# Optimization experiments

Measured on AMD Instinct MI355X. Metric: run time of the kernel, lower is better.

The kernel has to match this reference:

```python
import jax, jax.numpy as jnp
import numpy as np

MARGIN = 0.3
EPS = 1e-12


def setup_inputs() -> dict:
    key = jax.random.key(0)
    k1, k2, k3 = jax.random.split(key, 3)
    B, D = 8192, 1024
    features = jax.random.normal(k1, (B, D), dtype=jnp.float32)
    labels = jax.random.randint(k2, (B,), 0, 100, dtype=jnp.int64)
    domain_labels = jax.random.randint(k3, (B,), 0, 2, dtype=jnp.int64)
    return {"features": features, "labels": labels, "domain_labels": domain_labels}


def reference(features, labels, domain_labels):
    # L2-normalize rows (F.normalize: x / max(||x||, eps))
    norm = jnp.maximum(jnp.linalg.norm(features, axis=1, keepdims=True), EPS)
    f = features / norm

    herb = domain_labels == 0   # [B] anchors
    field = domain_labels == 1  # [B] candidates

    sq = jnp.sum(f * f, axis=1)                                   # [B]
    d2 = sq[:, None] + sq[None, :] - 2.0 * jnp.einsum('id,jd->ij', f, f)
    d = jnp.sqrt(jnp.maximum(d2, 0.0))                            # [B, B]

    same = labels[:, None] == labels[None, :]                     # [B, B]
    pair = herb[:, None] & field[None, :]
    pos_mask = pair & same
    neg_mask = pair & ~same

    INF = jnp.float32(jnp.inf)
    pos_min = jnp.min(jnp.where(pos_mask, d, INF), axis=1)        # [B]
    neg_min = jnp.min(jnp.where(neg_mask, d, INF), axis=1)        # [B]

    valid = herb & jnp.any(pos_mask, axis=1) & jnp.any(neg_mask, axis=1)
    # Substitute 0 for invalid rows BEFORE subtracting to avoid inf - inf.
    pos_s = jnp.where(valid, pos_min, 0.0)
    neg_s = jnp.where(valid, neg_min, 0.0)
    tl = jnp.maximum(pos_s - neg_s + MARGIN, 0.0)                 # [B]

    loss_sum = jnp.sum(jnp.where(valid, tl, 0.0))
    count = jnp.sum(valid.astype(jnp.float32))
    return jnp.where(count > 0, loss_sum / jnp.maximum(count, 1.0), 0.0)
```

## Files before the change

kernel.cpp:

```cpp
#include <hip/hip_runtime.h>


#define B_ROWS 8192
#define DIM    1024

typedef __bf16 bf16x8 __attribute__((ext_vector_type(8)));
typedef float  f32x4  __attribute__((ext_vector_type(4)));

__device__ __forceinline__ unsigned short f2bf_rne(float x) {
    unsigned u = __float_as_uint(x);
    unsigned r = (u + 0x7FFFu + ((u >> 16) & 1u)) >> 16;
    return (unsigned short)r;
}
__device__ __forceinline__ float bf2f(unsigned short h) {
    return __uint_as_float(((unsigned)h) << 16);
}

__device__ __forceinline__ void async_copy16(const void* g, void* l) {
    __builtin_amdgcn_global_load_lds(
        (const __attribute__((address_space(1))) unsigned int*)g,
        (__attribute__((address_space(3))) unsigned int*)l,
        16, 0, 0);
}

__global__ __launch_bounds__(256) void compute_slots(
    const int* __restrict__ dom, int* __restrict__ slotOf,
    unsigned* __restrict__ cnt)
{
    __shared__ int cnts[256];
    __shared__ int base[257];
    const int t = threadIdx.x;
    const int p0 = t * 32;

    unsigned mask = 0u; int c = 0;
    #pragma unroll
    for (int i = 0; i < 32; ++i) {
        const int isA = (dom[p0 + i] == 0) ? 1 : 0;
        mask |= ((unsigned)isA) << i;
        c += isA;
    }
    cnts[t] = c;
    __syncthreads();
    if (t == 0) {
        int acc = 0;
        for (int i = 0; i < 256; ++i) { base[i] = acc; acc += cnts[i]; }
        base[256] = acc;
        cnt[0] = (unsigned)acc;
    }
    __syncthreads();
    const int nA = base[256];
    int aB = base[t];
    #pragma unroll
    for (int i = 0; i < 32; ++i) {
        const int isA = (mask >> i) & 1;
        slotOf[p0 + i] = isA ? aB : nA + (p0 + i - aB);
        aB += isA;
    }
}

__global__ __launch_bounds__(256) void normalize_rows(
    const float* __restrict__ feat, const int* __restrict__ labels,
    const int* __restrict__ slotOf, unsigned short* __restrict__ G,
    int* __restrict__ labG, float* __restrict__ sqG)
{
    const int wv = threadIdx.x >> 6, lane = threadIdx.x & 63;
    const int row = blockIdx.x * 4 + wv;

    const float4* src = (const float4*)(feat + (size_t)row * DIM);
    float4 v[4];
    float ss = 0.0f;
    #pragma unroll
    for (int j = 0; j < 4; ++j) {
        v[j] = src[j * 64 + lane];
        ss += v[j].x * v[j].x + v[j].y * v[j].y + v[j].z * v[j].z + v[j].w * v[j].w;
    }
    #pragma unroll
    for (int s = 32; s > 0; s >>= 1) ss += __shfl_xor(ss, s);
    const float inv = 1.0f / fmaxf(sqrtf(ss), 1e-12f);

    const int slot = slotOf[row];
    unsigned short ub[16];
    float ss2 = 0.0f;
    #pragma unroll
    for (int j = 0; j < 4; ++j) {
        const float f0 = v[j].x * inv, f1 = v[j].y * inv,
                    f2 = v[j].z * inv, f3 = v[j].w * inv;
        ub[j * 4 + 0] = f2bf_rne(f0); ub[j * 4 + 1] = f2bf_rne(f1);
        ub[j * 4 + 2] = f2bf_rne(f2); ub[j * 4 + 3] = f2bf_rne(f3);
        #pragma unroll
        for (int q = 0; q < 4; ++q) {
            const float fr = bf2f(ub[j * 4 + q]);
            ss2 += fr * fr;
        }
    }
    #pragma unroll
    for (int s = 32; s > 0; s >>= 1) ss2 += __shfl_xor(ss2, s);
    if (lane == 0) {
        sqG[slot]  = ss2;
        labG[slot] = labels[row];
    }
    ushort4* dst = (ushort4*)(G + (size_t)slot * DIM);
    #pragma unroll
    for (int j = 0; j < 4; ++j) {
        ushort4 pk;
        pk.x = ub[j * 4 + 0]; pk.y = ub[j * 4 + 1];
        pk.z = ub[j * 4 + 2]; pk.w = ub[j * 4 + 3];
        dst[j * 64 + lane] = pk;
    }
}

__global__ __launch_bounds__(256) void tile_mindist(
    const unsigned short* __restrict__ G, const int* __restrict__ labG,
    const float* __restrict__ sqG, const unsigned* __restrict__ cnt,
    unsigned* __restrict__ posmin, unsigned* __restrict__ negmin)
{
    const int nA = (int)cnt[0];
    const int nF = B_ROWS - nA;
    const int nTA = (nA + 127) >> 7;
    const int nTF = (nF + 127) >> 7;
    const int total = nTA * nTF;

    __shared__ __align__(16) unsigned short S[2][2][128 * 32];

    const int t = threadIdx.x;
    const int lane = t & 63, w = t >> 6;
    const int wm = w >> 1, wn = w & 1;
    const int l15 = lane & 15, quad = lane >> 4;

    const int ch0 = 2 * w;
    const int crow = lane >> 2;
    const int cbyte = (lane & 3) * 16;

    const int rdA = (wm * 64 + l15) * 32 + quad * 8;
    const int rdF = (wn * 64 + l15) * 32 + quad * 8;

    const char* Gb = (const char*)G;

    for (int tile = blockIdx.x; tile < total; tile += gridDim.x) {
        const int tx = tile % nTA;
        const int ty = tile / nTA;
        const int rowA0 = tx * 128;
        const int rowF0 = nA + ty * 128;

        const char* ga[2]; const char* gf[2];
        #pragma unroll
        for (int h = 0; h < 2; ++h) {
            const int ch = ch0 + h;
            const int rA = rowA0 + 16 * ch + crow;
            int rF = rowF0 + 16 * ch + crow;
            if (rF > B_ROWS - 1) rF = B_ROWS - 1;
            ga[h] = Gb + (size_t)rA * (DIM * 2) + cbyte;
            gf[h] = Gb + (size_t)rF * (DIM * 2) + cbyte;
        }

        f32x4 acc[4][4] = {};

        #pragma unroll
        for (int h = 0; h < 2; ++h) {
            async_copy16(ga[h], &S[0][0][(ch0 + h) * 512]);
            async_copy16(gf[h], &S[0][1][(ch0 + h) * 512]);
        }
        __syncthreads();

        #pragma unroll 4
        for (int step = 0; step < 32; ++step) {
            const int cur = step & 1;
            const int nb = cur ^ 1;
            if (step < 31) {
                const int off = (step + 1) * 64;
                #pragma unroll
                for (int h = 0; h < 2; ++h) {
                    async_copy16(ga[h] + off, &S[nb][0][(ch0 + h) * 512]);
                    async_copy16(gf[h] + off, &S[nb][1][(ch0 + h) * 512]);
                }
            }

            const unsigned short* pa = &S[cur][0][rdA];
            const unsigned short* pf = &S[cur][1][rdF];
            bf16x8 a[4], b[4];
            #pragma unroll
            for (int fm = 0; fm < 4; ++fm) a[fm] = *(const bf16x8*)(pa + fm * 512);
            #pragma unroll
            for (int fn = 0; fn < 4; ++fn) b[fn] = *(const bf16x8*)(pf + fn * 512);
            #pragma unroll
            for (int fm = 0; fm < 4; ++fm)
                #pragma unroll
                for (int fn = 0; fn < 4; ++fn)
                    acc[fm][fn] = __builtin_amdgcn_mfma_f32_16x16x32_bf16(
                        a[fm], b[fn], acc[fm][fn], 0, 0, 0);

            __syncthreads();
        }

        const float INFV = __uint_as_float(0x7f800000u);
        float sqf[4]; int lf_[4]; bool vf[4];
        #pragma unroll
        for (int fn = 0; fn < 4; ++fn) {
            const int rf = rowF0 + wn * 64 + fn * 16 + l15;
            vf[fn] = rf < B_ROWS;
            const int rc = vf[fn] ? rf : (B_ROWS - 1);
            sqf[fn] = sqG[rc];
            lf_[fn] = labG[rc];
        }
        #pragma unroll
        for (int fm = 0; fm < 4; ++fm) {
            #pragma unroll
            for (int r = 0; r < 4; ++r) {
                const int ra = rowA0 + wm * 64 + fm * 16 + quad * 4 + r;
                const bool va = ra < nA;
                const int rac = va ? ra : 0;
                const float sqa = sqG[rac];
                const int la_ = labG[rac];
                float pmin = INFV, nmin = INFV;
                #pragma unroll
                for (int fn = 0; fn < 4; ++fn) {
                    const float dd = fmaxf(sqa + sqf[fn] - 2.0f * acc[fm][fn][r], 0.0f);
                    if (vf[fn]) {
                        if (la_ == lf_[fn]) pmin = fminf(pmin, dd);
                        else                nmin = fminf(nmin, dd);
                    }
                }
                #pragma unroll
                for (int s = 1; s < 16; s <<= 1) {
                    pmin = fminf(pmin, __shfl_xor(pmin, s));
                    nmin = fminf(nmin, __shfl_xor(nmin, s));
                }
                if (l15 == 0 && va) {
                    if (pmin < INFV) atomicMin(&posmin[ra], __float_as_uint(pmin));
                    if (nmin < INFV) atomicMin(&negmin[ra], __float_as_uint(nmin));
                }
            }
        }
        __syncthreads();
    }
}

__global__ __launch_bounds__(256) void reduce_loss(
    const unsigned* __restrict__ posmin, const unsigned* __restrict__ negmin,
    float* __restrict__ accum)
{
    const int i = blockIdx.x * 256 + threadIdx.x;
    const unsigned up = posmin[i], un = negmin[i];
    float tl = 0.0f, c = 0.0f;
    if (up != 0xFFFFFFFFu && un != 0xFFFFFFFFu) {
        const float pd = sqrtf(__uint_as_float(up));
        const float nd = sqrtf(__uint_as_float(un));
        tl = fmaxf(pd - nd + 0.3f, 0.0f);
        c = 1.0f;
    }
    #pragma unroll
    for (int s = 32; s > 0; s >>= 1) {
        tl += __shfl_down(tl, s);
        c  += __shfl_down(c, s);
    }
    __shared__ float sb[8];
    const int lane = threadIdx.x & 63, w = threadIdx.x >> 6;
    if (lane == 0) { sb[w] = tl; sb[4 + w] = c; }
    __syncthreads();
    if (threadIdx.x == 0) {
        atomicAdd(&accum[0], sb[0] + sb[1] + sb[2] + sb[3]);
        atomicAdd(&accum[1], sb[4] + sb[5] + sb[6] + sb[7]);
    }
}

__global__ void finalize(const float* __restrict__ accum, float* __restrict__ out) {
    const float s = accum[0], c = accum[1];
    out[0] = (c > 0.0f) ? s / fmaxf(c, 1.0f) : 0.0f;
}

extern "C" void kernel_launch(void* const* d_in, const int* in_sizes, int n_in,
                              void* d_out, int out_size, void* d_ws, size_t ws_size,
                              hipStream_t stream) {
    const float* feat  = (const float*)d_in[0];
    const int* labels  = (const int*)d_in[1];
    const int* dom     = (const int*)d_in[2];
    float* out = (float*)d_out;

    char* ws = (char*)d_ws;
    unsigned short* G   = (unsigned short*)(ws);
    int*      labG      = (int*)(ws + 16777216);
    float*    sqG       = (float*)(ws + 16809984);
    unsigned* posmin    = (unsigned*)(ws + 16842752);
    unsigned* negmin    = (unsigned*)(ws + 16875520);
    unsigned* cnt       = (unsigned*)(ws + 16908288);
    float*    accum     = (float*)(ws + 16908296);
    int*      slotOf    = (int*)(ws + 16842752);

    hipMemsetAsync(cnt, 0, 16, stream);

    compute_slots<<<1, 256, 0, stream>>>(dom, slotOf, cnt);
    normalize_rows<<<B_ROWS / 4, 256, 0, stream>>>(feat, labels, slotOf,
                                                   G, labG, sqG);

    hipMemsetAsync(posmin, 0xFF, 65536, stream);

    tile_mindist<<<1056, 256, 0, stream>>>(G, labG, sqG, cnt, posmin, negmin);

    reduce_loss<<<B_ROWS / 256, 256, 0, stream>>>(posmin, negmin, accum);
    finalize<<<1, 1, 0, stream>>>(accum, out);
}
```

Measured before the change: 179.1 us.

## Fold memsets and finalize into kernels, parallelize slot scan, XCD-aware tile mapping

Removes the two memset calls and the finalize launch. Buffer initialization moves into compute_slots and normalize_rows, and the final division happens in the last reduce_loss block through a ticket counter. The serial prefix sum in compute_slots becomes a wave-level shuffle scan with strided dom access. tile_mindist now gives each XCD (blockIdx & 7) a contiguous 2x4 sub-grid of tiles, so the A/F rows it touches stay in that XCD's L2. The risks are the new global ticket synchronization and slotOf aliasing posmin while being overwritten in place.

```diff
diff --git a/kernel.cpp b/kernel.cpp
--- a/kernel.cpp
+++ b/kernel.cpp
@@ -25,43 +25,62 @@
 
 __global__ __launch_bounds__(256) void compute_slots(
     const int* __restrict__ dom, int* __restrict__ slotOf,
-    unsigned* __restrict__ cnt)
+    unsigned* __restrict__ cnt, float* __restrict__ accum)
 {
     __shared__ int cnts[256];
     __shared__ int base[257];
     const int t = threadIdx.x;
-    const int p0 = t * 32;
+
+    if (t == 0) {
+        cnt[1] = 0u;
+        accum[0] = 0.0f;
+        accum[1] = 0.0f;
+    }
 
     unsigned mask = 0u; int c = 0;
     #pragma unroll
     for (int i = 0; i < 32; ++i) {
-        const int isA = (dom[p0 + i] == 0) ? 1 : 0;
+        const int isA = (dom[t + 256 * i] == 0) ? 1 : 0;
         mask |= ((unsigned)isA) << i;
         c += isA;
     }
     cnts[t] = c;
     __syncthreads();
-    if (t == 0) {
-        int acc = 0;
-        for (int i = 0; i < 256; ++i) { base[i] = acc; acc += cnts[i]; }
-        base[256] = acc;
-        cnt[0] = (unsigned)acc;
+    if (t < 64) {
+        const int c0 = cnts[4 * t + 0], c1 = cnts[4 * t + 1];
+        const int c2 = cnts[4 * t + 2], c3 = cnts[4 * t + 3];
+        const int s4 = c0 + c1 + c2 + c3;
+        int sc = s4;
+        #pragma unroll
+        for (int d = 1; d < 64; d <<= 1) {
+            const int o = __shfl_up(sc, d);
+            if (t >= d) sc += o;
+        }
+        const int b = sc - s4;
+        base[4 * t + 0] = b;
+        base[4 * t + 1] = b + c0;
+        base[4 * t + 2] = b + c0 + c1;
+        base[4 * t + 3] = b + c0 + c1 + c2;
+        if (t == 63) { base[256] = sc; cnt[0] = (unsigned)sc; }
     }
     __syncthreads();
     const int nA = base[256];
     int aB = base[t];
+    int fB = nA + t * 32 - base[t];
     #pragma unroll
     for (int i = 0; i < 32; ++i) {
         const int isA = (mask >> i) & 1;
-        slotOf[p0 + i] = isA ? aB : nA + (p0 + i - aB);
+        slotOf[t + 256 * i] = isA ? aB : fB;
         aB += isA;
+        fB += 1 - isA;
     }
 }
 
 __global__ __launch_bounds__(256) void normalize_rows(
     const float* __restrict__ feat, const int* __restrict__ labels,
-    const int* __restrict__ slotOf, unsigned short* __restrict__ G,
-    int* __restrict__ labG, float* __restrict__ sqG)
+    int* slotOf , unsigned* __restrict__ negmin,
+    unsigned short* __restrict__ G, int* __restrict__ labG,
+    float* __restrict__ sqG)
 {
     const int wv = threadIdx.x >> 6, lane = threadIdx.x & 63;
     const int row = blockIdx.x * 4 + wv;
@@ -79,6 +98,10 @@
     const float inv = 1.0f / fmaxf(sqrtf(ss), 1e-12f);
 
     const int slot = slotOf[row];
+    if (lane == 0) {
+        ((unsigned*)slotOf)[row] = 0xFFFFFFFFu;
+        negmin[row] = 0xFFFFFFFFu;
+    }
     unsigned short ub[16];
     float ss2 = 0.0f;
     #pragma unroll
@@ -118,7 +141,6 @@
     const int nF = B_ROWS - nA;
     const int nTA = (nA + 127) >> 7;
     const int nTF = (nF + 127) >> 7;
-    const int total = nTA * nTF;
 
     __shared__ __align__(16) unsigned short S[2][2][128 * 32];
 
@@ -136,9 +158,22 @@
 
     const char* Gb = (const char*)G;
 
-    for (int tile = blockIdx.x; tile < total; tile += gridDim.x) {
-        const int tx = tile % nTA;
-        const int ty = tile / nTA;
+    const int xcd = blockIdx.x & 7;
+    const int bx  = xcd & 1;
+    const int by  = xcd >> 1;
+    const int qa = nTA >> 1, ra = nTA & 1;
+    const int sa = qa + ((bx < ra) ? 1 : 0);
+    const int xa = bx * qa + ((bx < ra) ? bx : ra);
+    const int qf = nTF >> 2, rf = nTF & 3;
+    const int sf = qf + ((by < rf) ? 1 : 0);
+    const int ya = by * qf + ((by < rf) ? by : rf);
+    const int localN = sa * sf;
+    const int j0 = blockIdx.x >> 3;
+    const int jstride = (int)(gridDim.x >> 3);
+
+    for (int j = j0; j < localN; j += jstride) {
+        const int tx = xa + j / sf;
+        const int ty = ya + j % sf;
         const int rowA0 = tx * 128;
         const int rowF0 = nA + ty * 128;
 
@@ -196,9 +231,9 @@
         float sqf[4]; int lf_[4]; bool vf[4];
         #pragma unroll
         for (int fn = 0; fn < 4; ++fn) {
-            const int rf = rowF0 + wn * 64 + fn * 16 + l15;
-            vf[fn] = rf < B_ROWS;
-            const int rc = vf[fn] ? rf : (B_ROWS - 1);
+            const int rf2 = rowF0 + wn * 64 + fn * 16 + l15;
+            vf[fn] = rf2 < B_ROWS;
+            const int rc = vf[fn] ? rf2 : (B_ROWS - 1);
             sqf[fn] = sqG[rc];
             lf_[fn] = labG[rc];
         }
@@ -237,7 +272,8 @@
 
 __global__ __launch_bounds__(256) void reduce_loss(
     const unsigned* __restrict__ posmin, const unsigned* __restrict__ negmin,
-    float* __restrict__ accum)
+    float* __restrict__ accum, unsigned* __restrict__ cnt,
+    float* __restrict__ out)
 {
     const int i = blockIdx.x * 256 + threadIdx.x;
     const unsigned up = posmin[i], un = negmin[i];
@@ -260,12 +296,15 @@
     if (threadIdx.x == 0) {
         atomicAdd(&accum[0], sb[0] + sb[1] + sb[2] + sb[3]);
         atomicAdd(&accum[1], sb[4] + sb[5] + sb[6] + sb[7]);
-    }
-}
-
-__global__ void finalize(const float* __restrict__ accum, float* __restrict__ out) {
-    const float s = accum[0], c = accum[1];
-    out[0] = (c > 0.0f) ? s / fmaxf(c, 1.0f) : 0.0f;
+        __threadfence();
+        const unsigned ticket = atomicAdd(&cnt[1], 1u);
+        if (ticket == 31u) {
+            __threadfence();
+            const float s2 = atomicAdd(&accum[0], 0.0f);
+            const float c2 = atomicAdd(&accum[1], 0.0f);
+            out[0] = (c2 > 0.0f) ? s2 / fmaxf(c2, 1.0f) : 0.0f;
+        }
+    }
 }
 
 extern "C" void kernel_launch(void* const* d_in, const int* in_sizes, int n_in,
@@ -286,16 +325,11 @@
     float*    accum     = (float*)(ws + 16908296);
     int*      slotOf    = (int*)(ws + 16842752);
 
-    hipMemsetAsync(cnt, 0, 16, stream);
-
-    compute_slots<<<1, 256, 0, stream>>>(dom, slotOf, cnt);
+    compute_slots<<<1, 256, 0, stream>>>(dom, slotOf, cnt, accum);
     normalize_rows<<<B_ROWS / 4, 256, 0, stream>>>(feat, labels, slotOf,
-                                                   G, labG, sqG);
-
-    hipMemsetAsync(posmin, 0xFF, 65536, stream);
+                                                   negmin, G, labG, sqG);
 
     tile_mindist<<<1056, 256, 0, stream>>>(G, labG, sqG, cnt, posmin, negmin);
 
-    reduce_loss<<<B_ROWS / 256, 256, 0, stream>>>(posmin, negmin, accum);
-    finalize<<<1, 1, 0, stream>>>(accum, out);
-}
+    reduce_loss<<<B_ROWS / 256, 256, 0, stream>>>(posmin, negmin, accum, cnt, out);
+}
```

Result: faster. 170.1 us (-5.0%).
